# Kernel tuning notes

Hardware: AMD Instinct MI355X
Metric: run time of the kernel (lower is better)

Reference implementation:

```python
import jax, jax.numpy as jnp
import numpy as np

B, Hh, Ww, C = 2, 56, 56, 256
NH = 8
MH = MW = 7
NQ = 15


def setup_inputs() -> dict:
    key = jax.random.key(0)
    ks = jax.random.split(key, 8)
    x = jax.random.normal(ks[0], (B, Hh, Ww, C), jnp.float32)
    clstoken = jax.random.normal(ks[1], (B, NQ, C), jnp.float32)
    WN = MH * MW                      # 49 image windows
    WinPix = (Hh // MH) * (Ww // MW)  # 64 pixels per window
    clsWin = -(-NQ // WinPix)         # ceil -> 1 extra cls window
    M = WN + clsWin                   # 50
    # sparse top-k style routing mask; cls rows/cols all True (as in BiLayer)
    mask = jax.random.bernoulli(ks[2], 0.1, (B, M, M))
    mask = mask.at[:, WN:, :].set(True).at[:, :, WN:].set(True)
    mask = mask | jnp.eye(M, dtype=bool)[None]
    Wqkv = jax.random.normal(ks[3], (C, 3 * C), jnp.float32) * (C ** -0.5)
    bqkv = jnp.zeros((3 * C,), jnp.float32)
    lepe_w = jax.random.normal(ks[4], (3, 3, 1, C), jnp.float32) * 0.1  # depthwise HWIO
    lepe_b = jnp.zeros((C,), jnp.float32)
    Wo = jax.random.normal(ks[5], (C, C), jnp.float32) * (C ** -0.5)
    bo = jnp.zeros((C,), jnp.float32)
    return dict(x=x, clstoken=clstoken, mask=mask, Wqkv=Wqkv, bqkv=bqkv,
                lepe_w=lepe_w, lepe_b=lepe_b, Wo=Wo, bo=bo, mask_h=MH, mask_w=MW)


def reference(x, clstoken, mask, Wqkv, bqkv, lepe_w, lepe_b, Wo, bo, mask_h, mask_w):
    Bb, H, W, Cc = x.shape
    Nq = clstoken.shape[1]
    Nh = NH
    Hd = Cc // Nh
    Win_h, Win_w = H // mask_h, W // mask_w
    WinPix = Win_h * Win_w
    S_img = H * W
    S = S_img + Nq
    scale = Cc ** -0.5

    qkv = x @ Wqkv + bqkv
    q, k, v = jnp.split(qkv, 3, axis=-1)
    qkv_c = clstoken @ Wqkv + bqkv
    qc, kc, vc = jnp.split(qkv_c, 3, axis=-1)

    # depthwise lepe conv on v (NHWC)
    lepe = jax.lax.conv_general_dilated(
        v, lepe_w, (1, 1), 'SAME',
        dimension_numbers=('NHWC', 'HWIO', 'NHWC'),
        feature_group_count=Cc) + lepe_b

    def win(t):  # [B,H,W,C] -> [B,Nh,(j i h w),Hd] window-major token order
        t = t.reshape(Bb, mask_h, Win_h, mask_w, Win_w, Nh, Hd)
        return t.transpose(0, 5, 1, 3, 2, 4, 6).reshape(Bb, Nh, S_img, Hd)

    def heads_c(t):  # [B,Nq,C] -> [B,Nh,Nq,Hd]
        return t.reshape(Bb, Nq, Nh, Hd).transpose(0, 2, 1, 3)

    q = jnp.concatenate([win(q), heads_c(qc)], axis=2)
    k = jnp.concatenate([win(k), heads_c(kc)], axis=2)
    v = jnp.concatenate([win(v), heads_c(vc)], axis=2)

    # token-level mask from window-level routing mask: mask[b, q//WinPix, kv//WinPix]
    win_id = jnp.arange(S) // WinPix
    tokmask = mask[:, win_id[:, None], win_id[None, :]]  # [B,S,S]

    logits = jnp.einsum('bnqd,bnkd->bnqk', q, k) * scale
    logits = jnp.where(tokmask[:, None], logits, jnp.float32(-1e9))
    attn = jax.nn.softmax(logits, axis=-1)
    out = jnp.einsum('bnqk,bnkd->bnqd', attn, v)

    cls_out = out[:, :, S_img:, :].transpose(0, 2, 1, 3).reshape(Bb, Nq, Cc)
    ximg = out[:, :, :S_img, :].reshape(Bb, Nh, mask_h, mask_w, Win_h, Win_w, Hd)
    ximg = ximg.transpose(0, 2, 4, 3, 5, 1, 6).reshape(Bb, H, W, Cc)

    x_out = (ximg + lepe) @ Wo + bo
    cls_out = cls_out @ Wo + bo
    return (x_out, cls_out)
```

## Files before the change

kernel.cpp:

```cpp
#include <hip/hip_runtime.h>
#include <hip/hip_bf16.h>
#include <math.h>

#define Bsz 2
#define NHd 8
#define HD 32
#define CC 256
#define Himg 56
#define Wimg 56
#define SIMG 3136
#define NQtok 15
#define SS 3151
#define SP 3200
#define NWIN 50
#define WN 49
#define MM 50
#define MROWS (Bsz*SP)
#define NROWS (Bsz*SS)

#define QSZ (Bsz*NHd*SP*HD)
#define VSPSZ (Bsz*SIMG*CC)
#define USZ (MROWS*CC)

typedef __attribute__((ext_vector_type(8))) short bf16x8;
typedef __attribute__((ext_vector_type(4))) float f32x4;

__device__ __forceinline__ short f2bf(float f) {
    __hip_bfloat16 h = __float2bfloat16(f);
    return *reinterpret_cast<short*>(&h);
}
__device__ __forceinline__ float bf2f(unsigned short s) {
    unsigned int u = ((unsigned int)s) << 16;
    return __uint_as_float(u);
}
__device__ __forceinline__ unsigned int pk2(float lo, float hi) {
    return ((unsigned int)(unsigned short)f2bf(hi) << 16)
         | (unsigned int)(unsigned short)f2bf(lo);
}
__device__ __forceinline__ bf16x8 cvt8(const float* p) {
    float4 a = *(const float4*)p, b = *(const float4*)(p + 4);
    bf16x8 o;
    o[0] = f2bf(a.x); o[1] = f2bf(a.y); o[2] = f2bf(a.z); o[3] = f2bf(a.w);
    o[4] = f2bf(b.x); o[5] = f2bf(b.y); o[6] = f2bf(b.z); o[7] = f2bf(b.w);
    return o;
}

__device__ __forceinline__ void stage_wt(const float* __restrict__ W, int ld,
                                         int n0, int tid, short (*Wl)[264]) {
    int n = tid & 63;
    #pragma unroll
    for (int i = 0; i < 8; i++) {
        int k0 = ((tid >> 6) + i * 4) * 8;
        bf16x8 o;
        #pragma unroll
        for (int j = 0; j < 8; j++) o[j] = f2bf(W[(long)(k0 + j) * ld + n0 + n]);
        *(bf16x8*)&Wl[n][k0] = o;
    }
}

__global__ __launch_bounds__(256, 2) void qkv_fused(
        const float* __restrict__ x, const float* __restrict__ cls,
        const float* __restrict__ Wqkv, const float* __restrict__ bqkv,
        short* __restrict__ Qbf, short* __restrict__ Kbf, short* __restrict__ Vtb,
        short* __restrict__ Vsp) {
    __shared__ __align__(16) short As[64][264];
    __shared__ __align__(16) short Wl[64][264];
    int tid = threadIdx.x;
    int w = tid >> 6, l = tid & 63, l15 = l & 15, hi = l >> 4;
    int rb = blockIdx.x, nb = blockIdx.y;
    int n0 = nb * 64;

    #pragma unroll
    for (int p = 0; p < 8; p++) {
        int r = p * 8 + (tid >> 5);
        int c8 = (tid & 31) * 8;
        int row = rb * 64 + r;
        int b = row / SP, tok = row % SP;
        bf16x8 o = {0, 0, 0, 0, 0, 0, 0, 0};
        const float* pp = nullptr;
        if (tok < SIMG)      pp = x + (long)(b * SIMG + tok) * CC + c8;
        else if (tok < SS)   pp = cls + (long)(b * NQtok + tok - SIMG) * CC + c8;
        if (pp) o = cvt8(pp);
        *(bf16x8*)&As[r][c8] = o;
    }
    stage_wt(Wqkv, 768, n0, tid, Wl);
    __syncthreads();

    f32x4 acc[4];
    #pragma unroll
    for (int t = 0; t < 4; t++) acc[t] = (f32x4){0.f, 0.f, 0.f, 0.f};
    #pragma unroll
    for (int k0 = 0; k0 < 256; k0 += 32) {
        bf16x8 a = *(const bf16x8*)&As[w * 16 + l15][k0 + hi * 8];
        #pragma unroll
        for (int t = 0; t < 4; t++) {
            bf16x8 bf = *(const bf16x8*)&Wl[t * 16 + l15][k0 + hi * 8];
            acc[t] = __builtin_amdgcn_mfma_f32_16x16x32_bf16(a, bf, acc[t], 0, 0, 0);
        }
    }
    float bias[4];
    #pragma unroll
    for (int t = 0; t < 4; t++) bias[t] = bqkv[n0 + t * 16 + l15];
    int which = nb >> 2;
    #pragma unroll
    for (int r = 0; r < 4; r++) {
        int row = rb * 64 + w * 16 + hi * 4 + r;
        int b = row / SP, tok = row % SP;
        int s;
        if (tok < SIMG) {
            int h = tok / Wimg, wq = tok % Wimg;
            s = (((h >> 3) * 7 + (wq >> 3)) << 6) | ((h & 7) << 3) | (wq & 7);
        } else s = tok;
        #pragma unroll
        for (int t = 0; t < 4; t++) {
            int n = n0 + t * 16 + l15;
            float v = acc[t][r] + bias[t];
            int cch = n & 255;
            int head = cch >> 5, d = cch & 31;
            long off = (((long)(b * NHd + head)) * SP + s) * HD + d;
            if (which == 0)      Qbf[off] = f2bf(v * 0.0625f);
            else if (which == 1) Kbf[off] = f2bf(v);
            else {
                short vb = f2bf(v);
                Vtb[(((long)(b * NHd + head)) * NWIN + (s >> 6)) * 2048
                    + d * 64 + (s & 63)] = vb;
                if (tok < SIMG) Vsp[(long)(b * SIMG + tok) * CC + cch] = vb;
            }
        }
    }
}

__global__ __launch_bounds__(256, 2) void attn_mfma(
        const short* __restrict__ Qbf, const short* __restrict__ Kbf,
        const short* __restrict__ Vtb, const short* __restrict__ Vsp,
        const float* __restrict__ lepe_w, const float* __restrict__ lepe_b,
        const unsigned char* __restrict__ raw,
        short* __restrict__ U) {
    __shared__ __align__(16) unsigned int Pl[4][16][36];
    __shared__ float Ls[4][16];
    __shared__ float MAcc[4][16][32];

    int qb = blockIdx.x % NWIN;
    int bh = blockIdx.x / NWIN;
    int b = bh >> 3, head = bh & 7;
    int tid = threadIdx.x;
    int w = tid >> 6;
    int l = tid & 63;
    int l15 = l & 15;
    int hi = l >> 4;
    bool is_cls = (qb == WN);
    int qrow0 = is_cls ? 0 : w * 16;

    bf16x8 qf = *(const bf16x8*)&Qbf[((long)bh * SP + qb * 64 + qrow0 + l15) * HD + hi * 8];

    f32x4 acc0 = {0.f, 0.f, 0.f, 0.f};
    f32x4 acc1 = {0.f, 0.f, 0.f, 0.f};
    float l_run = 0.f;

    unsigned long long bits;
    if (!is_cls) {
        bool isbool = (raw[2453] | raw[2457] | raw[2461]) != 0;
        bool mv = false;
        long e = (long)b * MM * MM + (long)qb * MM + l;
        if (isbool) {
            if (l < NWIN) mv = raw[e] != 0;
        } else {
            if (l < NWIN) mv = ((const unsigned int*)raw)[e] != 0;
        }
        bits = __ballot(l < NWIN && mv);
    } else {
        bits = (0x1111111111111ULL << w) & ((1ULL << 50) - 1);
    }

    int kb = __builtin_ctzll(bits);
    bits &= bits - 1;
    const short* Kp = Kbf + ((long)bh * SP + kb * 64) * HD + hi * 8;
    bf16x8 kc0 = *(const bf16x8*)(Kp + (0 * 16 + l15) * HD);
    bf16x8 kc1 = *(const bf16x8*)(Kp + (1 * 16 + l15) * HD);
    bf16x8 kc2 = *(const bf16x8*)(Kp + (2 * 16 + l15) * HD);
    bf16x8 kc3 = *(const bf16x8*)(Kp + (3 * 16 + l15) * HD);

    for (;;) {
        long kbase = ((long)bh * SP + kb * 64) * HD;
        const short* Vp = Vtb + kbase;
        bf16x8 va = *(const bf16x8*)&Vp[l15 * 64 + hi * 8];
        bf16x8 vb = *(const bf16x8*)&Vp[(16 + l15) * 64 + hi * 8];
        bf16x8 vc = *(const bf16x8*)&Vp[l15 * 64 + 32 + hi * 8];
        bf16x8 vd = *(const bf16x8*)&Vp[(16 + l15) * 64 + 32 + hi * 8];

        f32x4 s[4];
        {
            f32x4 z = {0.f, 0.f, 0.f, 0.f};
            s[0] = __builtin_amdgcn_mfma_f32_16x16x32_bf16(kc0, qf, z, 0, 0, 0);
            s[1] = __builtin_amdgcn_mfma_f32_16x16x32_bf16(kc1, qf, z, 0, 0, 0);
            s[2] = __builtin_amdgcn_mfma_f32_16x16x32_bf16(kc2, qf, z, 0, 0, 0);
            s[3] = __builtin_amdgcn_mfma_f32_16x16x32_bf16(kc3, qf, z, 0, 0, 0);
        }
        if (kb == WN) {
            #pragma unroll
            for (int t = 0; t < 4; t++)
                #pragma unroll
                for (int r = 0; r < 4; r++)
                    if (t * 16 + hi * 4 + r >= NQtok) s[t][r] = -1e30f;
        }

        int nkb = -1;
        bf16x8 kn0, kn1, kn2, kn3;
        if (bits) {
            nkb = __builtin_ctzll(bits);
            bits &= bits - 1;
            const short* Kn = Kbf + ((long)bh * SP + nkb * 64) * HD + hi * 8;
            kn0 = *(const bf16x8*)(Kn + (0 * 16 + l15) * HD);
            kn1 = *(const bf16x8*)(Kn + (1 * 16 + l15) * HD);
            kn2 = *(const bf16x8*)(Kn + (2 * 16 + l15) * HD);
            kn3 = *(const bf16x8*)(Kn + (3 * 16 + l15) * HD);
        }

        float ps = 0.f;
        #pragma unroll
        for (int t = 0; t < 4; t++) {
            #pragma unroll
            for (int r = 0; r < 4; r++) {
                float p = __expf(fminf(s[t][r], 30.f));
                s[t][r] = p;
                ps += p;
            }
        }
        l_run += ps;

        #pragma unroll
        for (int t = 0; t < 4; t++) {
            uint2 pw;
            pw.x = pk2(s[t][0], s[t][1]);
            pw.y = pk2(s[t][2], s[t][3]);
            *(uint2*)&Pl[w][l15][t * 8 + hi * 2] = pw;
        }
        bf16x8 pb0 = *(const bf16x8*)&Pl[w][l15][hi * 4];
        bf16x8 pb1 = *(const bf16x8*)&Pl[w][l15][16 + hi * 4];

        acc0 = __builtin_amdgcn_mfma_f32_16x16x32_bf16(va, pb0, acc0, 0, 0, 0);
        acc1 = __builtin_amdgcn_mfma_f32_16x16x32_bf16(vb, pb0, acc1, 0, 0, 0);
        acc0 = __builtin_amdgcn_mfma_f32_16x16x32_bf16(vc, pb1, acc0, 0, 0, 0);
        acc1 = __builtin_amdgcn_mfma_f32_16x16x32_bf16(vd, pb1, acc1, 0, 0, 0);

        if (nkb < 0) break;
        kb = nkb;
        kc0 = kn0; kc1 = kn1; kc2 = kn2; kc3 = kn3;
    }

    float lsum = l_run;
    lsum += __shfl_xor(lsum, 16);
    lsum += __shfl_xor(lsum, 32);

    if (!is_cls) {
        float inv = 1.f / lsum;
        int wh = (qb / 7) * 8, wwc = (qb % 7) * 8;
        int inner = w * 16 + l15;
        int h0 = wh + (inner >> 3), w0 = wwc + (inner & 7);
        int c0 = head * HD + hi * 4;
        float u0[4], u1[4];
        #pragma unroll
        for (int r = 0; r < 4; r++) {
            u0[r] = acc0[r] * inv + lepe_b[c0 + r];
            u1[r] = acc1[r] * inv + lepe_b[c0 + 16 + r];
        }
        #pragma unroll
        for (int dh = -1; dh <= 1; dh++) {
            int h2 = h0 + dh;
            if (h2 < 0 || h2 >= Himg) continue;
            #pragma unroll
            for (int dw = -1; dw <= 1; dw++) {
                int w2 = w0 + dw;
                if (w2 < 0 || w2 >= Wimg) continue;
                long vbase = ((long)b * SIMG + h2 * Wimg + w2) * CC;
                int j = (dh + 1) * 3 + (dw + 1);
                ushort4 v0 = *(const ushort4*)&Vsp[vbase + c0];
                ushort4 v1 = *(const ushort4*)&Vsp[vbase + c0 + 16];
                float4 g0 = *(const float4*)&lepe_w[j * CC + c0];
                float4 g1 = *(const float4*)&lepe_w[j * CC + c0 + 16];
                u0[0] += bf2f(v0.x) * g0.x; u0[1] += bf2f(v0.y) * g0.y;
                u0[2] += bf2f(v0.z) * g0.z; u0[3] += bf2f(v0.w) * g0.w;
                u1[0] += bf2f(v1.x) * g1.x; u1[1] += bf2f(v1.y) * g1.y;
                u1[2] += bf2f(v1.z) * g1.z; u1[3] += bf2f(v1.w) * g1.w;
            }
        }
        long ubase = ((long)(b * SS + h0 * Wimg + w0)) * CC + c0;
        ushort4 o0, o1;
        o0.x = (unsigned short)f2bf(u0[0]); o0.y = (unsigned short)f2bf(u0[1]);
        o0.z = (unsigned short)f2bf(u0[2]); o0.w = (unsigned short)f2bf(u0[3]);
        o1.x = (unsigned short)f2bf(u1[0]); o1.y = (unsigned short)f2bf(u1[1]);
        o1.z = (unsigned short)f2bf(u1[2]); o1.w = (unsigned short)f2bf(u1[3]);
        *(ushort4*)&U[ubase]      = o0;
        *(ushort4*)&U[ubase + 16] = o1;
    } else {
        if (hi == 0) Ls[w][l15] = lsum;
        #pragma unroll
        for (int r = 0; r < 4; r++) {
            MAcc[w][l15][hi * 4 + r]      = acc0[r];
            MAcc[w][l15][16 + hi * 4 + r] = acc1[r];
        }
        __syncthreads();
        if (w == 0) {
            float L = Ls[0][l15] + Ls[1][l15] + Ls[2][l15] + Ls[3][l15];
            float o0[4] = {0.f, 0.f, 0.f, 0.f}, o1[4] = {0.f, 0.f, 0.f, 0.f};
            #pragma unroll
            for (int ww = 0; ww < 4; ww++) {
                #pragma unroll
                for (int r = 0; r < 4; r++) {
                    o0[r] += MAcc[ww][l15][hi * 4 + r];
                    o1[r] += MAcc[ww][l15][16 + hi * 4 + r];
                }
            }
            if (l15 < NQtok) {
                float invL = 1.f / L;
                long ubase = ((long)(b * SS + SIMG + l15)) * CC + head * HD + hi * 4;
                ushort4 q0, q1;
                q0.x = (unsigned short)f2bf(o0[0] * invL);
                q0.y = (unsigned short)f2bf(o0[1] * invL);
                q0.z = (unsigned short)f2bf(o0[2] * invL);
                q0.w = (unsigned short)f2bf(o0[3] * invL);
                q1.x = (unsigned short)f2bf(o1[0] * invL);
                q1.y = (unsigned short)f2bf(o1[1] * invL);
                q1.z = (unsigned short)f2bf(o1[2] * invL);
                q1.w = (unsigned short)f2bf(o1[3] * invL);
                *(ushort4*)&U[ubase]      = q0;
                *(ushort4*)&U[ubase + 16] = q1;
            }
        }
    }
}

__global__ __launch_bounds__(256, 2) void out_fused(
        const short* __restrict__ U, const float* __restrict__ Wo,
        const float* __restrict__ bo, float* __restrict__ out) {
    __shared__ __align__(16) short Wl[64][264];
    int tid = threadIdx.x;
    int w = tid >> 6, l = tid & 63, l15 = l & 15, hi = l >> 4;
    int row0 = blockIdx.x * 128 + w * 32;
    int n0 = blockIdx.y * 64;

    stage_wt(Wo, 256, n0, tid, Wl);
    __syncthreads();

    f32x4 acc[2][4];
    #pragma unroll
    for (int rs = 0; rs < 2; rs++)
        #pragma unroll
        for (int t = 0; t < 4; t++) acc[rs][t] = (f32x4){0.f, 0.f, 0.f, 0.f};
    const short* Ap0 = U + (long)(row0 + l15) * CC + hi * 8;
    const short* Ap1 = Ap0 + 16 * CC;
    #pragma unroll
    for (int k0 = 0; k0 < 256; k0 += 32) {
        bf16x8 a0 = *(const bf16x8*)(Ap0 + k0);
        bf16x8 a1 = *(const bf16x8*)(Ap1 + k0);
        #pragma unroll
        for (int t = 0; t < 4; t++) {
            bf16x8 bf = *(const bf16x8*)&Wl[t * 16 + l15][k0 + hi * 8];
            acc[0][t] = __builtin_amdgcn_mfma_f32_16x16x32_bf16(a0, bf, acc[0][t], 0, 0, 0);
            acc[1][t] = __builtin_amdgcn_mfma_f32_16x16x32_bf16(a1, bf, acc[1][t], 0, 0, 0);
        }
    }
    float bias[4];
    #pragma unroll
    for (int t = 0; t < 4; t++) bias[t] = bo[n0 + t * 16 + l15];
    #pragma unroll
    for (int rs = 0; rs < 2; rs++) {
        #pragma unroll
        for (int r = 0; r < 4; r++) {
            int row = row0 + rs * 16 + hi * 4 + r;
            if (row >= NROWS) continue;
            int b = (row >= SS) ? 1 : 0;
            int tok = row - b * SS;
            long base;
            if (tok < SIMG) base = (long)(b * SIMG + tok) * CC;
            else base = (long)Bsz * SIMG * CC + (long)(b * NQtok + tok - SIMG) * CC;
            #pragma unroll
            for (int t = 0; t < 4; t++)
                out[base + n0 + t * 16 + l15] = acc[rs][t][r] + bias[t];
        }
    }
}

extern "C" void kernel_launch(void* const* d_in, const int* in_sizes, int n_in,
                              void* d_out, int out_size, void* d_ws, size_t ws_size,
                              hipStream_t stream) {
    const float* x      = (const float*)d_in[0];
    const float* cls    = (const float*)d_in[1];
    const unsigned char* mask_raw = (const unsigned char*)d_in[2];
    const float* Wqkv   = (const float*)d_in[3];
    const float* bqkv   = (const float*)d_in[4];
    const float* lepe_w = (const float*)d_in[5];
    const float* lepe_b = (const float*)d_in[6];
    const float* Wo     = (const float*)d_in[7];
    const float* bo     = (const float*)d_in[8];
    float* out = (float*)d_out;

    short* Qbf = (short*)d_ws;
    short* Kbf = Qbf + QSZ;
    short* Vtb = Kbf + QSZ;
    short* U   = Vtb + QSZ;
    short* Vsp = U + USZ;

    qkv_fused<<<dim3(MROWS / 64, 12), 256, 0, stream>>>(x, cls, Wqkv, bqkv, Qbf, Kbf, Vtb, Vsp);
    attn_mfma<<<Bsz * NHd * NWIN, 256, 0, stream>>>(Qbf, Kbf, Vtb, Vsp, lepe_w, lepe_b, mask_raw, U);
    out_fused<<<dim3(MROWS / 128, 4), 256, 0, stream>>>(U, Wo, bo, out);
}
```

Measured before the change: 69.43 us.

## Fuse output projection into attention kernel via per-head split-K atomics

Removes the separate out-projection kernel and the U intermediate buffer. Each attention block multiplies its per-head 32-channel slice by the matching Wo rows with MFMA and atomically adds into the output, which the QKV kernel now zero-fills beforehand. Each head adds bias/8 so the eight contributions sum to the full bias. This saves one launch and the U round trip through memory, but adds many fp32 global atomics, the zeroing writes, and a per-block restaging of a Wo slice with scalar strided loads.

```diff
diff --git a/kernel.cpp b/kernel.cpp
--- a/kernel.cpp
+++ b/kernel.cpp
@@ -20,7 +20,7 @@
 
 #define QSZ (Bsz*NHd*SP*HD)
 #define VSPSZ (Bsz*SIMG*CC)
-#define USZ (MROWS*CC)
+#define OUTF4 ((NROWS*CC)/4)
 
 typedef __attribute__((ext_vector_type(8))) short bf16x8;
 typedef __attribute__((ext_vector_type(4))) float f32x4;
@@ -45,30 +45,24 @@
     return o;
 }
 
-__device__ __forceinline__ void stage_wt(const float* __restrict__ W, int ld,
-                                         int n0, int tid, short (*Wl)[264]) {
-    int n = tid & 63;
-    #pragma unroll
-    for (int i = 0; i < 8; i++) {
-        int k0 = ((tid >> 6) + i * 4) * 8;
-        bf16x8 o;
-        #pragma unroll
-        for (int j = 0; j < 8; j++) o[j] = f2bf(W[(long)(k0 + j) * ld + n0 + n]);
-        *(bf16x8*)&Wl[n][k0] = o;
-    }
-}
-
 __global__ __launch_bounds__(256, 2) void qkv_fused(
         const float* __restrict__ x, const float* __restrict__ cls,
         const float* __restrict__ Wqkv, const float* __restrict__ bqkv,
         short* __restrict__ Qbf, short* __restrict__ Kbf, short* __restrict__ Vtb,
-        short* __restrict__ Vsp) {
+        short* __restrict__ Vsp, float4* __restrict__ outz) {
     __shared__ __align__(16) short As[64][264];
     __shared__ __align__(16) short Wl[64][264];
     int tid = threadIdx.x;
     int w = tid >> 6, l = tid & 63, l15 = l & 15, hi = l >> 4;
     int rb = blockIdx.x, nb = blockIdx.y;
     int n0 = nb * 64;
+
+    {
+        int gid = (rb * 12 + nb) * 256 + tid;
+        float4 z = {0.f, 0.f, 0.f, 0.f};
+        if (gid < OUTF4) outz[gid] = z;
+        if (gid + 307200 < OUTF4) outz[gid + 307200] = z;
+    }
 
     #pragma unroll
     for (int p = 0; p < 8; p++) {
@@ -83,7 +77,17 @@
         if (pp) o = cvt8(pp);
         *(bf16x8*)&As[r][c8] = o;
     }
-    stage_wt(Wqkv, 768, n0, tid, Wl);
+    {
+        int n = tid & 63;
+        #pragma unroll
+        for (int i = 0; i < 8; i++) {
+            int k0 = ((tid >> 6) + i * 4) * 8;
+            bf16x8 o;
+            #pragma unroll
+            for (int j = 0; j < 8; j++) o[j] = f2bf(Wqkv[(long)(k0 + j) * 768 + n0 + n]);
+            *(bf16x8*)&Wl[n][k0] = o;
+        }
+    }
     __syncthreads();
 
     f32x4 acc[4];
@@ -130,15 +134,18 @@
     }
 }
 
-__global__ __launch_bounds__(256, 2) void attn_mfma(
+__global__ __launch_bounds__(256, 2) void attn_out(
         const short* __restrict__ Qbf, const short* __restrict__ Kbf,
         const short* __restrict__ Vtb, const short* __restrict__ Vsp,
         const float* __restrict__ lepe_w, const float* __restrict__ lepe_b,
         const unsigned char* __restrict__ raw,
-        short* __restrict__ U) {
+        const float* __restrict__ Wo, const float* __restrict__ bo,
+        float* __restrict__ out) {
     __shared__ __align__(16) unsigned int Pl[4][16][36];
     __shared__ float Ls[4][16];
     __shared__ float MAcc[4][16][32];
+    __shared__ __align__(16) short Wl[256][40];
+    __shared__ __align__(16) short Ul[4][16][40];
 
     int qb = blockIdx.x % NWIN;
     int bh = blockIdx.x / NWIN;
@@ -151,6 +158,10 @@
     bool is_cls = (qb == WN);
     int qrow0 = is_cls ? 0 : w * 16;
 
+    for (int k = 0; k < 32; k++)
+        Wl[tid][k] = f2bf(Wo[(long)(head * 32 + k) * CC + tid]);
+    __syncthreads();
+
     bf16x8 qf = *(const bf16x8*)&Qbf[((long)bh * SP + qb * 64 + qrow0 + l15) * HD + hi * 8];
 
     f32x4 acc0 = {0.f, 0.f, 0.f, 0.f};
@@ -252,6 +263,7 @@
     lsum += __shfl_xor(lsum, 16);
     lsum += __shfl_xor(lsum, 32);
 
+    bool do_out = true;
     if (!is_cls) {
         float inv = 1.f / lsum;
         int wh = (qb / 7) * 8, wwc = (qb % 7) * 8;
@@ -284,14 +296,11 @@
                 u1[2] += bf2f(v1.z) * g1.z; u1[3] += bf2f(v1.w) * g1.w;
             }
         }
-        long ubase = ((long)(b * SS + h0 * Wimg + w0)) * CC + c0;
-        ushort4 o0, o1;
-        o0.x = (unsigned short)f2bf(u0[0]); o0.y = (unsigned short)f2bf(u0[1]);
-        o0.z = (unsigned short)f2bf(u0[2]); o0.w = (unsigned short)f2bf(u0[3]);
-        o1.x = (unsigned short)f2bf(u1[0]); o1.y = (unsigned short)f2bf(u1[1]);
-        o1.z = (unsigned short)f2bf(u1[2]); o1.w = (unsigned short)f2bf(u1[3]);
-        *(ushort4*)&U[ubase]      = o0;
-        *(ushort4*)&U[ubase + 16] = o1;
+        unsigned int* Urow = (unsigned int*)&Ul[w][l15][0];
+        Urow[hi * 2]     = pk2(u0[0], u0[1]);
+        Urow[hi * 2 + 1] = pk2(u0[2], u0[3]);
+        Urow[8 + hi * 2]     = pk2(u1[0], u1[1]);
+        Urow[8 + hi * 2 + 1] = pk2(u1[2], u1[3]);
     } else {
         if (hi == 0) Ls[w][l15] = lsum;
         #pragma unroll
@@ -300,7 +309,8 @@
             MAcc[w][l15][16 + hi * 4 + r] = acc1[r];
         }
         __syncthreads();
-        if (w == 0) {
+        do_out = (w == 0);
+        if (do_out) {
             float L = Ls[0][l15] + Ls[1][l15] + Ls[2][l15] + Ls[3][l15];
             float o0[4] = {0.f, 0.f, 0.f, 0.f}, o1[4] = {0.f, 0.f, 0.f, 0.f};
             #pragma unroll
@@ -311,72 +321,38 @@
                     o1[r] += MAcc[ww][l15][16 + hi * 4 + r];
                 }
             }
-            if (l15 < NQtok) {
-                float invL = 1.f / L;
-                long ubase = ((long)(b * SS + SIMG + l15)) * CC + head * HD + hi * 4;
-                ushort4 q0, q1;
-                q0.x = (unsigned short)f2bf(o0[0] * invL);
-                q0.y = (unsigned short)f2bf(o0[1] * invL);
-                q0.z = (unsigned short)f2bf(o0[2] * invL);
-                q0.w = (unsigned short)f2bf(o0[3] * invL);
-                q1.x = (unsigned short)f2bf(o1[0] * invL);
-                q1.y = (unsigned short)f2bf(o1[1] * invL);
-                q1.z = (unsigned short)f2bf(o1[2] * invL);
-                q1.w = (unsigned short)f2bf(o1[3] * invL);
-                *(ushort4*)&U[ubase]      = q0;
-                *(ushort4*)&U[ubase + 16] = q1;
-            }
-        }
-    }
-}
-
-__global__ __launch_bounds__(256, 2) void out_fused(
-        const short* __restrict__ U, const float* __restrict__ Wo,
-        const float* __restrict__ bo, float* __restrict__ out) {
-    __shared__ __align__(16) short Wl[64][264];
-    int tid = threadIdx.x;
-    int w = tid >> 6, l = tid & 63, l15 = l & 15, hi = l >> 4;
-    int row0 = blockIdx.x * 128 + w * 32;
-    int n0 = blockIdx.y * 64;
-
-    stage_wt(Wo, 256, n0, tid, Wl);
-    __syncthreads();
-
-    f32x4 acc[2][4];
-    #pragma unroll
-    for (int rs = 0; rs < 2; rs++)
-        #pragma unroll
-        for (int t = 0; t < 4; t++) acc[rs][t] = (f32x4){0.f, 0.f, 0.f, 0.f};
-    const short* Ap0 = U + (long)(row0 + l15) * CC + hi * 8;
-    const short* Ap1 = Ap0 + 16 * CC;
-    #pragma unroll
-    for (int k0 = 0; k0 < 256; k0 += 32) {
-        bf16x8 a0 = *(const bf16x8*)(Ap0 + k0);
-        bf16x8 a1 = *(const bf16x8*)(Ap1 + k0);
-        #pragma unroll
-        for (int t = 0; t < 4; t++) {
-            bf16x8 bf = *(const bf16x8*)&Wl[t * 16 + l15][k0 + hi * 8];
-            acc[0][t] = __builtin_amdgcn_mfma_f32_16x16x32_bf16(a0, bf, acc[0][t], 0, 0, 0);
-            acc[1][t] = __builtin_amdgcn_mfma_f32_16x16x32_bf16(a1, bf, acc[1][t], 0, 0, 0);
-        }
-    }
-    float bias[4];
-    #pragma unroll
-    for (int t = 0; t < 4; t++) bias[t] = bo[n0 + t * 16 + l15];
-    #pragma unroll
-    for (int rs = 0; rs < 2; rs++) {
-        #pragma unroll
-        for (int r = 0; r < 4; r++) {
-            int row = row0 + rs * 16 + hi * 4 + r;
-            if (row >= NROWS) continue;
-            int b = (row >= SS) ? 1 : 0;
-            int tok = row - b * SS;
-            long base;
-            if (tok < SIMG) base = (long)(b * SIMG + tok) * CC;
-            else base = (long)Bsz * SIMG * CC + (long)(b * NQtok + tok - SIMG) * CC;
-            #pragma unroll
-            for (int t = 0; t < 4; t++)
-                out[base + n0 + t * 16 + l15] = acc[rs][t][r] + bias[t];
+            float invL = 1.f / L;
+            unsigned int* Urow = (unsigned int*)&Ul[0][l15][0];
+            Urow[hi * 2]     = pk2(o0[0] * invL, o0[1] * invL);
+            Urow[hi * 2 + 1] = pk2(o0[2] * invL, o0[3] * invL);
+            Urow[8 + hi * 2]     = pk2(o1[0] * invL, o1[1] * invL);
+            Urow[8 + hi * 2 + 1] = pk2(o1[2] * invL, o1[3] * invL);
+        }
+    }
+
+    if (do_out) {
+        bf16x8 ua = *(const bf16x8*)&Ul[w][l15][hi * 8];
+        int wh = (qb / 7) * 8, wwc = (qb % 7) * 8;
+        #pragma unroll
+        for (int t = 0; t < 16; t++) {
+            float bv = bo[t * 16 + l15] * 0.125f;
+            f32x4 c = {bv, bv, bv, bv};
+            bf16x8 bt = *(const bf16x8*)&Wl[t * 16 + l15][hi * 8];
+            c = __builtin_amdgcn_mfma_f32_16x16x32_bf16(ua, bt, c, 0, 0, 0);
+            #pragma unroll
+            for (int r = 0; r < 4; r++) {
+                int qrow = hi * 4 + r;
+                long base;
+                if (!is_cls) {
+                    int inner = w * 16 + qrow;
+                    int tok = (wh + (inner >> 3)) * Wimg + wwc + (inner & 7);
+                    base = ((long)(b * SIMG) + tok) * CC;
+                } else {
+                    if (qrow >= NQtok) continue;
+                    base = (long)Bsz * SIMG * CC + ((long)(b * NQtok + qrow)) * CC;
+                }
+                atomicAdd(&out[base + t * 16 + l15], c[r]);
+            }
         }
     }
 }
@@ -398,10 +374,10 @@
     short* Qbf = (short*)d_ws;
     short* Kbf = Qbf + QSZ;
     short* Vtb = Kbf + QSZ;
-    short* U   = Vtb + QSZ;
-    short* Vsp = U + USZ;
-
-    qkv_fused<<<dim3(MROWS / 64, 12), 256, 0, stream>>>(x, cls, Wqkv, bqkv, Qbf, Kbf, Vtb, Vsp);
-    attn_mfma<<<Bsz * NHd * NWIN, 256, 0, stream>>>(Qbf, Kbf, Vtb, Vsp, lepe_w, lepe_b, mask_raw, U);
-    out_fused<<<dim3(MROWS / 128, 4), 256, 0, stream>>>(U, Wo, bo, out);
-}
+    short* Vsp = Vtb + QSZ;
+
+    qkv_fused<<<dim3(MROWS / 64, 12), 256, 0, stream>>>(
+        x, cls, Wqkv, bqkv, Qbf, Kbf, Vtb, Vsp, (float4*)out);
+    attn_out<<<Bsz * NHd * NWIN, 256, 0, stream>>>(
+        Qbf, Kbf, Vtb, Vsp, lepe_w, lepe_b, mask_raw, Wo, bo, out);
+}
```

Result: slower. 101.1 us (+45.7%).

## Pre-transpose Wo to bf16 in QKV kernel, swizzle block order for XCD locality

Applied to the files above, without the earlier changes.

The Wo weight is now transposed and converted to bf16 once, by a few blocks of the QKV kernel, into a workspace buffer. The output GEMM reads its B fragments directly from global memory, dropping the strided per-block fp32 staging into LDS and the sync that went with it. Both the QKV and attention grids get a block-index swizzle so that neighbouring tiles land on the same XCD and share L2. The cost is extra workspace, a slightly longer tail on the QKV kernel, and uncoalesced-by-LDS global B loads in the output GEMM.

```diff
diff --git a/kernel.cpp b/kernel.cpp
--- a/kernel.cpp
+++ b/kernel.cpp
@@ -21,6 +21,7 @@
 #define QSZ (Bsz*NHd*SP*HD)
 #define VSPSZ (Bsz*SIMG*CC)
 #define USZ (MROWS*CC)
+#define WOTSZ (CC*CC)
 
 typedef __attribute__((ext_vector_type(8))) short bf16x8;
 typedef __attribute__((ext_vector_type(4))) float f32x4;
@@ -45,29 +46,18 @@
     return o;
 }
 
-__device__ __forceinline__ void stage_wt(const float* __restrict__ W, int ld,
-                                         int n0, int tid, short (*Wl)[264]) {
-    int n = tid & 63;
-    #pragma unroll
-    for (int i = 0; i < 8; i++) {
-        int k0 = ((tid >> 6) + i * 4) * 8;
-        bf16x8 o;
-        #pragma unroll
-        for (int j = 0; j < 8; j++) o[j] = f2bf(W[(long)(k0 + j) * ld + n0 + n]);
-        *(bf16x8*)&Wl[n][k0] = o;
-    }
-}
-
 __global__ __launch_bounds__(256, 2) void qkv_fused(
         const float* __restrict__ x, const float* __restrict__ cls,
         const float* __restrict__ Wqkv, const float* __restrict__ bqkv,
+        const float* __restrict__ Wo,
         short* __restrict__ Qbf, short* __restrict__ Kbf, short* __restrict__ Vtb,
-        short* __restrict__ Vsp) {
+        short* __restrict__ Vsp, short* __restrict__ Wot) {
     __shared__ __align__(16) short As[64][264];
     __shared__ __align__(16) short Wl[64][264];
     int tid = threadIdx.x;
     int w = tid >> 6, l = tid & 63, l15 = l & 15, hi = l >> 4;
-    int rb = blockIdx.x, nb = blockIdx.y;
+    int t0 = (blockIdx.x & 7) * 150 + (blockIdx.x >> 3);
+    int rb = t0 / 12, nb = t0 % 12;
     int n0 = nb * 64;
 
     #pragma unroll
@@ -83,7 +73,17 @@
         if (pp) o = cvt8(pp);
         *(bf16x8*)&As[r][c8] = o;
     }
-    stage_wt(Wqkv, 768, n0, tid, Wl);
+    {
+        int n = tid & 63;
+        #pragma unroll
+        for (int i = 0; i < 8; i++) {
+            int k0 = ((tid >> 6) + i * 4) * 8;
+            bf16x8 o;
+            #pragma unroll
+            for (int j = 0; j < 8; j++) o[j] = f2bf(Wqkv[(long)(k0 + j) * 768 + n0 + n]);
+            *(bf16x8*)&Wl[n][k0] = o;
+        }
+    }
     __syncthreads();
 
     f32x4 acc[4];
@@ -128,6 +128,24 @@
             }
         }
     }
+
+    if (nb == 0 && rb < 16) {
+        __syncthreads();
+        float (*tile)[65] = (float (*)[65])As;
+        int k0 = (rb & 3) * 64, n0w = (rb >> 2) * 64;
+        int c = tid & 63, r0 = tid >> 6;
+        #pragma unroll
+        for (int p = 0; p < 16; p++) {
+            int kl = p * 4 + r0;
+            tile[kl][c] = Wo[(long)(k0 + kl) * CC + n0w + c];
+        }
+        __syncthreads();
+        #pragma unroll
+        for (int p = 0; p < 16; p++) {
+            int nl = p * 4 + r0;
+            Wot[(long)(n0w + nl) * CC + k0 + c] = f2bf(tile[c][nl]);
+        }
+    }
 }
 
 __global__ __launch_bounds__(256, 2) void attn_mfma(
@@ -140,8 +158,9 @@
     __shared__ float Ls[4][16];
     __shared__ float MAcc[4][16][32];
 
-    int qb = blockIdx.x % NWIN;
-    int bh = blockIdx.x / NWIN;
+    int swz = (blockIdx.x & 7) * 100 + (blockIdx.x >> 3);
+    int qb = swz % NWIN;
+    int bh = swz / NWIN;
     int b = bh >> 3, head = bh & 7;
     int tid = threadIdx.x;
     int w = tid >> 6;
@@ -330,18 +349,13 @@
     }
 }
 
-__global__ __launch_bounds__(256, 2) void out_fused(
-        const short* __restrict__ U, const float* __restrict__ Wo,
+__global__ __launch_bounds__(256, 2) void out_gemm_mfma(
+        const short* __restrict__ U, const short* __restrict__ Wot,
         const float* __restrict__ bo, float* __restrict__ out) {
-    __shared__ __align__(16) short Wl[64][264];
     int tid = threadIdx.x;
     int w = tid >> 6, l = tid & 63, l15 = l & 15, hi = l >> 4;
     int row0 = blockIdx.x * 128 + w * 32;
     int n0 = blockIdx.y * 64;
-
-    stage_wt(Wo, 256, n0, tid, Wl);
-    __syncthreads();
-
     f32x4 acc[2][4];
     #pragma unroll
     for (int rs = 0; rs < 2; rs++)
@@ -349,13 +363,14 @@
         for (int t = 0; t < 4; t++) acc[rs][t] = (f32x4){0.f, 0.f, 0.f, 0.f};
     const short* Ap0 = U + (long)(row0 + l15) * CC + hi * 8;
     const short* Ap1 = Ap0 + 16 * CC;
+    const short* Bp = Wot + (long)(n0 + l15) * CC + hi * 8;
     #pragma unroll
     for (int k0 = 0; k0 < 256; k0 += 32) {
         bf16x8 a0 = *(const bf16x8*)(Ap0 + k0);
         bf16x8 a1 = *(const bf16x8*)(Ap1 + k0);
         #pragma unroll
         for (int t = 0; t < 4; t++) {
-            bf16x8 bf = *(const bf16x8*)&Wl[t * 16 + l15][k0 + hi * 8];
+            bf16x8 bf = *(const bf16x8*)(Bp + t * 16 * CC + k0);
             acc[0][t] = __builtin_amdgcn_mfma_f32_16x16x32_bf16(a0, bf, acc[0][t], 0, 0, 0);
             acc[1][t] = __builtin_amdgcn_mfma_f32_16x16x32_bf16(a1, bf, acc[1][t], 0, 0, 0);
         }
@@ -400,8 +415,11 @@
     short* Vtb = Kbf + QSZ;
     short* U   = Vtb + QSZ;
     short* Vsp = U + USZ;
-
-    qkv_fused<<<dim3(MROWS / 64, 12), 256, 0, stream>>>(x, cls, Wqkv, bqkv, Qbf, Kbf, Vtb, Vsp);
-    attn_mfma<<<Bsz * NHd * NWIN, 256, 0, stream>>>(Qbf, Kbf, Vtb, Vsp, lepe_w, lepe_b, mask_raw, U);
-    out_fused<<<dim3(MROWS / 128, 4), 256, 0, stream>>>(U, Wo, bo, out);
-}
+    short* Wot = Vsp + VSPSZ;
+
+    qkv_fused<<<1200, 256, 0, stream>>>(
+        x, cls, Wqkv, bqkv, Wo, Qbf, Kbf, Vtb, Vsp, Wot);
+    attn_mfma<<<Bsz * NHd * NWIN, 256, 0, stream>>>(
+        Qbf, Kbf, Vtb, Vsp, lepe_w, lepe_b, mask_raw, U);
+    out_gemm_mfma<<<dim3(MROWS / 128, 4), 256, 0, stream>>>(U, Wot, bo, out);
+}
```

Result: no change. 70.58 us (+1.6%).

## Split attention key blocks across two wave groups per query strip

Applied to the files above, without the earlier changes.

The attention kernel now launches 512 threads per block. Each 16-row query strip gets two waves that take alternating active key blocks from the routing mask, and their partial accumulators and row sums are merged through shared memory before the lepe/output epilogue. The cls block spreads its key blocks over eight waves instead of four. This shortens the serial per-wave loop over key blocks to hide latency, at the cost of an extra block barrier, more shared memory, and half the waves idling during the epilogue.

```diff
diff --git a/kernel.cpp b/kernel.cpp
--- a/kernel.cpp
+++ b/kernel.cpp
@@ -130,26 +130,30 @@
     }
 }
 
-__global__ __launch_bounds__(256, 2) void attn_mfma(
+__global__ __launch_bounds__(512, 2) void attn_mfma(
         const short* __restrict__ Qbf, const short* __restrict__ Kbf,
         const short* __restrict__ Vtb, const short* __restrict__ Vsp,
         const float* __restrict__ lepe_w, const float* __restrict__ lepe_b,
         const unsigned char* __restrict__ raw,
         short* __restrict__ U) {
-    __shared__ __align__(16) unsigned int Pl[4][16][36];
-    __shared__ float Ls[4][16];
-    __shared__ float MAcc[4][16][32];
+    __shared__ __align__(16) unsigned int Pl[8][16][36];
+    __shared__ float MrgA[4][64][8];
+    __shared__ float MrgL[4][64];
+    __shared__ float Ls[8][16];
+    __shared__ float MAcc[8][16][32];
 
     int qb = blockIdx.x % NWIN;
     int bh = blockIdx.x / NWIN;
     int b = bh >> 3, head = bh & 7;
     int tid = threadIdx.x;
     int w = tid >> 6;
+    int strip = w & 3;
+    int sel = w >> 2;
     int l = tid & 63;
     int l15 = l & 15;
     int hi = l >> 4;
     bool is_cls = (qb == WN);
-    int qrow0 = is_cls ? 0 : w * 16;
+    int qrow0 = is_cls ? 0 : strip * 16;
 
     bf16x8 qf = *(const bf16x8*)&Qbf[((long)bh * SP + qb * 64 + qrow0 + l15) * HD + hi * 8];
 
@@ -157,7 +161,7 @@
     f32x4 acc1 = {0.f, 0.f, 0.f, 0.f};
     float l_run = 0.f;
 
-    unsigned long long bits;
+    unsigned long long mine = 0;
     if (!is_cls) {
         bool isbool = (raw[2453] | raw[2457] | raw[2461]) != 0;
         bool mv = false;
@@ -167,95 +171,133 @@
         } else {
             if (l < NWIN) mv = ((const unsigned int*)raw)[e] != 0;
         }
-        bits = __ballot(l < NWIN && mv);
+        unsigned long long bits = __ballot(l < NWIN && mv);
+        int idx = 0;
+        while (bits) {
+            int k = __builtin_ctzll(bits);
+            bits &= bits - 1;
+            if ((idx & 1) == sel) mine |= 1ULL << k;
+            idx++;
+        }
     } else {
-        bits = (0x1111111111111ULL << w) & ((1ULL << 50) - 1);
-    }
-
-    int kb = __builtin_ctzll(bits);
-    bits &= bits - 1;
-    const short* Kp = Kbf + ((long)bh * SP + kb * 64) * HD + hi * 8;
-    bf16x8 kc0 = *(const bf16x8*)(Kp + (0 * 16 + l15) * HD);
-    bf16x8 kc1 = *(const bf16x8*)(Kp + (1 * 16 + l15) * HD);
-    bf16x8 kc2 = *(const bf16x8*)(Kp + (2 * 16 + l15) * HD);
-    bf16x8 kc3 = *(const bf16x8*)(Kp + (3 * 16 + l15) * HD);
-
-    for (;;) {
-        long kbase = ((long)bh * SP + kb * 64) * HD;
-        const short* Vp = Vtb + kbase;
-        bf16x8 va = *(const bf16x8*)&Vp[l15 * 64 + hi * 8];
-        bf16x8 vb = *(const bf16x8*)&Vp[(16 + l15) * 64 + hi * 8];
-        bf16x8 vc = *(const bf16x8*)&Vp[l15 * 64 + 32 + hi * 8];
-        bf16x8 vd = *(const bf16x8*)&Vp[(16 + l15) * 64 + 32 + hi * 8];
-
-        f32x4 s[4];
-        {
-            f32x4 z = {0.f, 0.f, 0.f, 0.f};
-            s[0] = __builtin_amdgcn_mfma_f32_16x16x32_bf16(kc0, qf, z, 0, 0, 0);
-            s[1] = __builtin_amdgcn_mfma_f32_16x16x32_bf16(kc1, qf, z, 0, 0, 0);
-            s[2] = __builtin_amdgcn_mfma_f32_16x16x32_bf16(kc2, qf, z, 0, 0, 0);
-            s[3] = __builtin_amdgcn_mfma_f32_16x16x32_bf16(kc3, qf, z, 0, 0, 0);
-        }
-        if (kb == WN) {
-            #pragma unroll
-            for (int t = 0; t < 4; t++)
+        mine = (0x0101010101010101ULL << w) & ((1ULL << 50) - 1);
+    }
+
+    if (mine) {
+        int kb = __builtin_ctzll(mine);
+        mine &= mine - 1;
+        const short* Kp = Kbf + ((long)bh * SP + kb * 64) * HD + hi * 8;
+        bf16x8 kc0 = *(const bf16x8*)(Kp + (0 * 16 + l15) * HD);
+        bf16x8 kc1 = *(const bf16x8*)(Kp + (1 * 16 + l15) * HD);
+        bf16x8 kc2 = *(const bf16x8*)(Kp + (2 * 16 + l15) * HD);
+        bf16x8 kc3 = *(const bf16x8*)(Kp + (3 * 16 + l15) * HD);
+
+        for (;;) {
+            long kbase = ((long)bh * SP + kb * 64) * HD;
+            const short* Vp = Vtb + kbase;
+            bf16x8 va = *(const bf16x8*)&Vp[l15 * 64 + hi * 8];
+            bf16x8 vb = *(const bf16x8*)&Vp[(16 + l15) * 64 + hi * 8];
+            bf16x8 vc = *(const bf16x8*)&Vp[l15 * 64 + 32 + hi * 8];
+            bf16x8 vd = *(const bf16x8*)&Vp[(16 + l15) * 64 + 32 + hi * 8];
+
+            f32x4 s[4];
+            {
+                f32x4 z = {0.f, 0.f, 0.f, 0.f};
+                s[0] = __builtin_amdgcn_mfma_f32_16x16x32_bf16(kc0, qf, z, 0, 0, 0);
+                s[1] = __builtin_amdgcn_mfma_f32_16x16x32_bf16(kc1, qf, z, 0, 0, 0);
+                s[2] = __builtin_amdgcn_mfma_f32_16x16x32_bf16(kc2, qf, z, 0, 0, 0);
+                s[3] = __builtin_amdgcn_mfma_f32_16x16x32_bf16(kc3, qf, z, 0, 0, 0);
+            }
+            if (kb == WN) {
                 #pragma unroll
-                for (int r = 0; r < 4; r++)
-                    if (t * 16 + hi * 4 + r >= NQtok) s[t][r] = -1e30f;
-        }
-
-        int nkb = -1;
-        bf16x8 kn0, kn1, kn2, kn3;
-        if (bits) {
-            nkb = __builtin_ctzll(bits);
-            bits &= bits - 1;
-            const short* Kn = Kbf + ((long)bh * SP + nkb * 64) * HD + hi * 8;
-            kn0 = *(const bf16x8*)(Kn + (0 * 16 + l15) * HD);
-            kn1 = *(const bf16x8*)(Kn + (1 * 16 + l15) * HD);
-            kn2 = *(const bf16x8*)(Kn + (2 * 16 + l15) * HD);
-            kn3 = *(const bf16x8*)(Kn + (3 * 16 + l15) * HD);
-        }
-
-        float ps = 0.f;
-        #pragma unroll
-        for (int t = 0; t < 4; t++) {
+                for (int t = 0; t < 4; t++)
+                    #pragma unroll
+                    for (int r = 0; r < 4; r++)
+                        if (t * 16 + hi * 4 + r >= NQtok) s[t][r] = -1e30f;
+            }
+
+            int nkb = -1;
+            bf16x8 kn0, kn1, kn2, kn3;
+            if (mine) {
+                nkb = __builtin_ctzll(mine);
+                mine &= mine - 1;
+                const short* Kn = Kbf + ((long)bh * SP + nkb * 64) * HD + hi * 8;
+                kn0 = *(const bf16x8*)(Kn + (0 * 16 + l15) * HD);
+                kn1 = *(const bf16x8*)(Kn + (1 * 16 + l15) * HD);
+                kn2 = *(const bf16x8*)(Kn + (2 * 16 + l15) * HD);
+                kn3 = *(const bf16x8*)(Kn + (3 * 16 + l15) * HD);
+            }
+
+            float ps = 0.f;
+            #pragma unroll
+            for (int t = 0; t < 4; t++) {
+                #pragma unroll
+                for (int r = 0; r < 4; r++) {
+                    float p = __expf(fminf(s[t][r], 30.f));
+                    s[t][r] = p;
+                    ps += p;
+                }
+            }
+            l_run += ps;
+
+            #pragma unroll
+            for (int t = 0; t < 4; t++) {
+                uint2 pw;
+                pw.x = pk2(s[t][0], s[t][1]);
+                pw.y = pk2(s[t][2], s[t][3]);
+                *(uint2*)&Pl[w][l15][t * 8 + hi * 2] = pw;
+            }
+            bf16x8 pb0 = *(const bf16x8*)&Pl[w][l15][hi * 4];
+            bf16x8 pb1 = *(const bf16x8*)&Pl[w][l15][16 + hi * 4];
+
+            acc0 = __builtin_amdgcn_mfma_f32_16x16x32_bf16(va, pb0, acc0, 0, 0, 0);
+            acc1 = __builtin_amdgcn_mfma_f32_16x16x32_bf16(vb, pb0, acc1, 0, 0, 0);
+            acc0 = __builtin_amdgcn_mfma_f32_16x16x32_bf16(vc, pb1, acc0, 0, 0, 0);
+            acc1 = __builtin_amdgcn_mfma_f32_16x16x32_bf16(vd, pb1, acc1, 0, 0, 0);
+
+            if (nkb < 0) break;
+            kb = nkb;
+            kc0 = kn0; kc1 = kn1; kc2 = kn2; kc3 = kn3;
+        }
+    }
+
+    if (!is_cls) {
+        if (sel == 1) {
             #pragma unroll
             for (int r = 0; r < 4; r++) {
-                float p = __expf(fminf(s[t][r], 30.f));
-                s[t][r] = p;
-                ps += p;
-            }
-        }
-        l_run += ps;
-
-        #pragma unroll
-        for (int t = 0; t < 4; t++) {
-            uint2 pw;
-            pw.x = pk2(s[t][0], s[t][1]);
-            pw.y = pk2(s[t][2], s[t][3]);
-            *(uint2*)&Pl[w][l15][t * 8 + hi * 2] = pw;
-        }
-        bf16x8 pb0 = *(const bf16x8*)&Pl[w][l15][hi * 4];
-        bf16x8 pb1 = *(const bf16x8*)&Pl[w][l15][16 + hi * 4];
-
-        acc0 = __builtin_amdgcn_mfma_f32_16x16x32_bf16(va, pb0, acc0, 0, 0, 0);
-        acc1 = __builtin_amdgcn_mfma_f32_16x16x32_bf16(vb, pb0, acc1, 0, 0, 0);
-        acc0 = __builtin_amdgcn_mfma_f32_16x16x32_bf16(vc, pb1, acc0, 0, 0, 0);
-        acc1 = __builtin_amdgcn_mfma_f32_16x16x32_bf16(vd, pb1, acc1, 0, 0, 0);
-
-        if (nkb < 0) break;
-        kb = nkb;
-        kc0 = kn0; kc1 = kn1; kc2 = kn2; kc3 = kn3;
-    }
-
-    float lsum = l_run;
-    lsum += __shfl_xor(lsum, 16);
-    lsum += __shfl_xor(lsum, 32);
+                MrgA[strip][l][r]     = acc0[r];
+                MrgA[strip][l][4 + r] = acc1[r];
+            }
+            MrgL[strip][l] = l_run;
+        }
+    } else {
+        float ws = l_run;
+        ws += __shfl_xor(ws, 16);
+        ws += __shfl_xor(ws, 32);
+        if (hi == 0) Ls[w][l15] = ws;
+        #pragma unroll
+        for (int r = 0; r < 4; r++) {
+            MAcc[w][l15][hi * 4 + r]      = acc0[r];
+            MAcc[w][l15][16 + hi * 4 + r] = acc1[r];
+        }
+    }
+    __syncthreads();
 
     if (!is_cls) {
+        if (sel != 0) return;
+        #pragma unroll
+        for (int r = 0; r < 4; r++) {
+            acc0[r] += MrgA[strip][l][r];
+            acc1[r] += MrgA[strip][l][4 + r];
+        }
+        l_run += MrgL[strip][l];
+        float lsum = l_run;
+        lsum += __shfl_xor(lsum, 16);
+        lsum += __shfl_xor(lsum, 32);
         float inv = 1.f / lsum;
+
         int wh = (qb / 7) * 8, wwc = (qb % 7) * 8;
-        int inner = w * 16 + l15;
+        int inner = strip * 16 + l15;
         int h0 = wh + (inner >> 3), w0 = wwc + (inner & 7);
         int c0 = head * HD + hi * 4;
         float u0[4], u1[4];
@@ -293,39 +335,33 @@
         *(ushort4*)&U[ubase]      = o0;
         *(ushort4*)&U[ubase + 16] = o1;
     } else {
-        if (hi == 0) Ls[w][l15] = lsum;
-        #pragma unroll
-        for (int r = 0; r < 4; r++) {
-            MAcc[w][l15][hi * 4 + r]      = acc0[r];
-            MAcc[w][l15][16 + hi * 4 + r] = acc1[r];
-        }
-        __syncthreads();
-        if (w == 0) {
-            float L = Ls[0][l15] + Ls[1][l15] + Ls[2][l15] + Ls[3][l15];
-            float o0[4] = {0.f, 0.f, 0.f, 0.f}, o1[4] = {0.f, 0.f, 0.f, 0.f};
-            #pragma unroll
-            for (int ww = 0; ww < 4; ww++) {
-                #pragma unroll
-                for (int r = 0; r < 4; r++) {
-                    o0[r] += MAcc[ww][l15][hi * 4 + r];
-                    o1[r] += MAcc[ww][l15][16 + hi * 4 + r];
-                }
-            }
-            if (l15 < NQtok) {
-                float invL = 1.f / L;
-                long ubase = ((long)(b * SS + SIMG + l15)) * CC + head * HD + hi * 4;
-                ushort4 q0, q1;
-                q0.x = (unsigned short)f2bf(o0[0] * invL);
-                q0.y = (unsigned short)f2bf(o0[1] * invL);
-                q0.z = (unsigned short)f2bf(o0[2] * invL);
-                q0.w = (unsigned short)f2bf(o0[3] * invL);
-                q1.x = (unsigned short)f2bf(o1[0] * invL);
-                q1.y = (unsigned short)f2bf(o1[1] * invL);
-                q1.z = (unsigned short)f2bf(o1[2] * invL);
-                q1.w = (unsigned short)f2bf(o1[3] * invL);
-                *(ushort4*)&U[ubase]      = q0;
-                *(ushort4*)&U[ubase + 16] = q1;
-            }
+        if (w != 0) return;
+        float L = 0.f;
+        #pragma unroll
+        for (int ww = 0; ww < 8; ww++) L += Ls[ww][l15];
+        float o0[4] = {0.f, 0.f, 0.f, 0.f}, o1[4] = {0.f, 0.f, 0.f, 0.f};
+        #pragma unroll
+        for (int ww = 0; ww < 8; ww++) {
+            #pragma unroll
+            for (int r = 0; r < 4; r++) {
+                o0[r] += MAcc[ww][l15][hi * 4 + r];
+                o1[r] += MAcc[ww][l15][16 + hi * 4 + r];
+            }
+        }
+        if (l15 < NQtok) {
+            float invL = 1.f / L;
+            long ubase = ((long)(b * SS + SIMG + l15)) * CC + head * HD + hi * 4;
+            ushort4 q0, q1;
+            q0.x = (unsigned short)f2bf(o0[0] * invL);
+            q0.y = (unsigned short)f2bf(o0[1] * invL);
+            q0.z = (unsigned short)f2bf(o0[2] * invL);
+            q0.w = (unsigned short)f2bf(o0[3] * invL);
+            q1.x = (unsigned short)f2bf(o1[0] * invL);
+            q1.y = (unsigned short)f2bf(o1[1] * invL);
+            q1.z = (unsigned short)f2bf(o1[2] * invL);
+            q1.w = (unsigned short)f2bf(o1[3] * invL);
+            *(ushort4*)&U[ubase]      = q0;
+            *(ushort4*)&U[ubase + 16] = q1;
         }
     }
 }
@@ -402,6 +438,6 @@
     short* Vsp = U + USZ;
 
     qkv_fused<<<dim3(MROWS / 64, 12), 256, 0, stream>>>(x, cls, Wqkv, bqkv, Qbf, Kbf, Vtb, Vsp);
-    attn_mfma<<<Bsz * NHd * NWIN, 256, 0, stream>>>(Qbf, Kbf, Vtb, Vsp, lepe_w, lepe_b, mask_raw, U);
+    attn_mfma<<<Bsz * NHd * NWIN, 512, 0, stream>>>(Qbf, Kbf, Vtb, Vsp, lepe_w, lepe_b, mask_raw, U);
     out_fused<<<dim3(MROWS / 128, 4), 256, 0, stream>>>(U, Wo, bo, out);
 }
```

Measured after the change: 69.55 us. No clear change (+0.2%).
